# Optimization experiments

Measured on AMD Instinct MI355X. Metric: run time of the kernel, lower is better.

The kernel has to match this reference:

```python
import jax, jax.numpy as jnp
import numpy as np

KSIZE = 3

def setup_inputs() -> dict:
    key = jax.random.key(0)
    k1, k2, k3, k4 = jax.random.split(key, 4)
    B, C, H, W = 4, 64, 256, 512
    x = jax.random.normal(k1, (B, C, H, W), dtype=jnp.float32)
    # precomputed latitude-dependent resampling index into flattened H*W
    idx_flat = jax.random.randint(k2, (KSIZE * H * KSIZE * W,), 0, H * W, dtype=jnp.int64)
    weight = jax.random.normal(k3, (C, C, KSIZE, KSIZE), dtype=jnp.float32) * 0.05
    bias = jax.random.normal(k4, (C,), dtype=jnp.float32) * 0.05
    return {"x": x, "idx_flat": idx_flat, "weight": weight, "bias": bias}

def reference(x, idx_flat, weight, bias):
    B, C, H, W = x.shape
    k = KSIZE
    # latitude-dependent scaled gather: [B, C, H*W] -> [B, C, k*H, k*W]
    x1d = x.reshape(B, C, H * W)
    scaled = jnp.take(x1d, idx_flat, axis=2).reshape(B, C, k * H, k * W)
    # conv with kernel=stride=k, no padding -> [B, C, H, W]
    out = jax.lax.conv_general_dilated(
        scaled, weight,
        window_strides=(k, k), padding='VALID',
        dimension_numbers=('NCHW', 'OIHW', 'NCHW'))
    return out + bias[None, :, None, None]
```

## Files before the change

### kernel.cpp

```cpp
#include <hip/hip_runtime.h>
#include <stdint.h>

#define HW_   131072
#define W_    512
#define C_    64
#define KDIM  576

typedef __bf16 bf16_t;
typedef bf16_t bf16x8 __attribute__((ext_vector_type(8)));
typedef float  f32x4_t __attribute__((ext_vector_type(4)));

__device__ __forceinline__ unsigned short f32_to_bf16(float f) {
    union { float f; unsigned u; } v; v.f = f;
    unsigned r = (v.u + 0x7FFFu + ((v.u >> 16) & 1u)) >> 16;
    return (unsigned short)r;
}

#define XT_BYTES   67108864ull
#define WF_BYTES   73728ull


__global__ __launch_bounds__(256) void k_prep_w(const float* __restrict__ w,
                                                unsigned short* __restrict__ wfrag) {
    int id = blockIdx.x * 256 + threadIdx.x;
    if (id >= 18 * 4 * 64) return;
    int lane = id & 63;
    int nt   = (id >> 6) & 3;
    int kc   = id >> 8;
    int n  = nt * 16 + (lane & 15);
    int k0 = kc * 32 + ((lane >> 4) << 3);
    unsigned short tmp[8];
#pragma unroll
    for (int j = 0; j < 8; ++j) {
        int k = k0 + j;
        int t = k >> 6;
        int c = k & 63;
        tmp[j] = f32_to_bf16(w[(size_t)n * KDIM + c * 9 + t]);
    }
    uint4 v;
    v.x = tmp[0] | ((unsigned)tmp[1] << 16);
    v.y = tmp[2] | ((unsigned)tmp[3] << 16);
    v.z = tmp[4] | ((unsigned)tmp[5] << 16);
    v.w = tmp[6] | ((unsigned)tmp[7] << 16);
    ((uint4*)wfrag)[id] = v;
}

__global__ __launch_bounds__(256) void k_transpose(const float* __restrict__ x,
                                                   unsigned short* __restrict__ xt) {
    int gp = blockIdx.x * 256 + threadIdx.x;
    int b = gp >> 17;
    int p = gp & (HW_ - 1);
    const float* xb = x + ((size_t)b * C_) * HW_ + p;
    uint4* dst = (uint4*)(xt + (size_t)gp * C_);
#pragma unroll
    for (int cc = 0; cc < 8; ++cc) {
        unsigned short tmp[8];
#pragma unroll
        for (int j = 0; j < 8; ++j)
            tmp[j] = f32_to_bf16(xb[(size_t)(cc * 8 + j) * HW_]);
        uint4 v;
        v.x = tmp[0] | ((unsigned)tmp[1] << 16);
        v.y = tmp[2] | ((unsigned)tmp[3] << 16);
        v.z = tmp[4] | ((unsigned)tmp[5] << 16);
        v.w = tmp[6] | ((unsigned)tmp[7] << 16);
        dst[cc] = v;
    }
}

__global__ __launch_bounds__(256) void k_gemm(const unsigned short* __restrict__ xt,
                                              const unsigned short* __restrict__ wfrag,
                                              const int* __restrict__ idx,
                                              const float* __restrict__ bias,
                                              float* __restrict__ out) {
    __shared__ unsigned p_lds[4][64][9];

    int tid  = threadIdx.x;
    int wave = tid >> 6;
    int lane = tid & 63;
    int gbase = blockIdx.x * 256 + wave * 64;
    int b = gbase >> 17;

    {
        int g  = gbase + lane;
        int hw = g & (HW_ - 1);
        int h = hw >> 9, w = hw & (W_ - 1);
        size_t base = (size_t)(3 * h) * (3 * W_) + 3 * w;
#pragma unroll
        for (int th = 0; th < 3; ++th)
#pragma unroll
            for (int tw = 0; tw < 3; ++tw)
                p_lds[wave][lane][th * 3 + tw] = (unsigned)idx[base + (size_t)th * (3 * W_) + tw];
    }
    __syncthreads();

    f32x4_t acc[4][4] = {};
    int quad = lane >> 4;
    int col  = lane & 15;
    const unsigned short* xtb = xt + (((size_t)b) << 17) * C_;

    for (int kc = 0; kc < 18; ++kc) {
        int t = kc >> 1;
        int byteoff = ((kc & 1) << 6) + (quad << 4);

        bf16x8 bfrag[4];
#pragma unroll
        for (int nt = 0; nt < 4; ++nt) {
            const uint4* wp = (const uint4*)(wfrag + ((size_t)((kc * 4 + nt) * 64 + lane) << 3));
            bfrag[nt] = __builtin_bit_cast(bf16x8, *wp);
        }
        bf16x8 afrag[4];
#pragma unroll
        for (int ms = 0; ms < 4; ++ms) {
            unsigned p = p_lds[wave][ms * 16 + col][t];
            const uint4* ap = (const uint4*)((const char*)(xtb + (size_t)p * C_) + byteoff);
            afrag[ms] = __builtin_bit_cast(bf16x8, *ap);
        }
#pragma unroll
        for (int ms = 0; ms < 4; ++ms)
#pragma unroll
            for (int nt = 0; nt < 4; ++nt)
                acc[ms][nt] = __builtin_amdgcn_mfma_f32_16x16x32_bf16(
                    afrag[ms], bfrag[nt], acc[ms][nt], 0, 0, 0);
    }

#pragma unroll
    for (int nt = 0; nt < 4; ++nt) {
        int o = nt * 16 + col;
        float bv = bias[o];
#pragma unroll
        for (int ms = 0; ms < 4; ++ms) {
            int m0 = ms * 16 + quad * 4;
            int hw0 = (gbase + m0) & (HW_ - 1);
            f32x4_t v = acc[ms][nt];
            v.x += bv; v.y += bv; v.z += bv; v.w += bv;
            *(f32x4_t*)(out + (((size_t)(b * 64 + o)) << 17) + hw0) = v;
        }
    }
}

__global__ __launch_bounds__(256) void k_fallback(const float* __restrict__ x,
                                                  const int* __restrict__ idx,
                                                  const float* __restrict__ w,
                                                  const float* __restrict__ bias,
                                                  float* __restrict__ out) {
    size_t g = (size_t)blockIdx.x * 256 + threadIdx.x;
    int hw = (int)(g & (HW_ - 1));
    int o  = (int)((g >> 17) & 63);
    int b  = (int)(g >> 23);
    int h = hw >> 9, ww = hw & (W_ - 1);
    size_t ibase = (size_t)(3 * h) * (3 * W_) + 3 * ww;
    int p[9];
#pragma unroll
    for (int th = 0; th < 3; ++th)
#pragma unroll
        for (int tw = 0; tw < 3; ++tw)
            p[th * 3 + tw] = idx[ibase + (size_t)th * (3 * W_) + tw];
    const float* xb = x + (size_t)b * C_ * HW_;
    const float* wo = w + (size_t)o * KDIM;
    float acc = bias[o];
    for (int c = 0; c < C_; ++c) {
        const float* xc = xb + (size_t)c * HW_;
        const float* wc = wo + c * 9;
#pragma unroll
        for (int t = 0; t < 9; ++t)
            acc += xc[p[t]] * wc[t];
    }
    out[g] = acc;
}

extern "C" void kernel_launch(void* const* d_in, const int* in_sizes, int n_in,
                              void* d_out, int out_size, void* d_ws, size_t ws_size,
                              hipStream_t stream) {
    const float* x    = (const float*)d_in[0];
    const int*   idx  = (const int*)d_in[1];
    const float* w    = (const float*)d_in[2];
    const float* bias = (const float*)d_in[3];
    float* out = (float*)d_out;

    if (ws_size >= XT_BYTES + WF_BYTES) {
        unsigned short* xt    = (unsigned short*)d_ws;
        unsigned short* wfrag = (unsigned short*)((char*)d_ws + XT_BYTES);
        k_prep_w   <<<18,   256, 0, stream>>>(w, wfrag);
        k_transpose<<<2048, 256, 0, stream>>>(x, xt);
        k_gemm     <<<2048, 256, 0, stream>>>(xt, wfrag, idx, bias, out);
    } else {
        k_fallback<<<131072, 256, 0, stream>>>(x, idx, w, bias, out);
    }
}
```

Measured before the change: 375.2 us.

## Stage transpose through LDS and software-pipeline gather loads in GEMM

The transpose kernel now stages a 256-pixel by 64-channel tile in shared memory, so the bf16 channel-last writes become contiguous 16-byte stores rather than strided per-thread stores. The gather-GEMM halves the rows per wave (32 pixels, 128 per block, twice as many blocks) to raise occupancy. It also software-pipelines the gathered A and weight B fragment loads three stages ahead with a fully unrolled K loop, and caches the indices in registers. The cost is more registers for the prefetch buffers, and less weight-fragment reuse per MFMA since each wave now does half as many MFMAs per B load.

```diff
diff --git a/kernel.cpp b/kernel.cpp
--- a/kernel.cpp
+++ b/kernel.cpp
@@ -18,7 +18,6 @@
 
 #define XT_BYTES   67108864ull
 #define WF_BYTES   73728ull
-
 
 __global__ __launch_bounds__(256) void k_prep_w(const float* __restrict__ w,
                                                 unsigned short* __restrict__ wfrag) {
@@ -47,23 +46,31 @@
 
 __global__ __launch_bounds__(256) void k_transpose(const float* __restrict__ x,
                                                    unsigned short* __restrict__ xt) {
-    int gp = blockIdx.x * 256 + threadIdx.x;
-    int b = gp >> 17;
-    int p = gp & (HW_ - 1);
-    const float* xb = x + ((size_t)b * C_) * HW_ + p;
-    uint4* dst = (uint4*)(xt + (size_t)gp * C_);
-#pragma unroll
-    for (int cc = 0; cc < 8; ++cc) {
-        unsigned short tmp[8];
-#pragma unroll
-        for (int j = 0; j < 8; ++j)
-            tmp[j] = f32_to_bf16(xb[(size_t)(cc * 8 + j) * HW_]);
+    __shared__ unsigned short tile[256][68];
+    int t  = threadIdx.x;
+    int gp0 = blockIdx.x * 256;
+    int b  = gp0 >> 17;
+    int p0 = gp0 & (HW_ - 1);
+    const float* xb = x + ((size_t)b * C_) * HW_ + p0 + t;
+#pragma unroll
+    for (int c = 0; c < 64; c += 2) {
+        unsigned a0 = f32_to_bf16(xb[(size_t)c << 17]);
+        unsigned a1 = f32_to_bf16(xb[(size_t)(c + 1) << 17]);
+        *(unsigned*)&tile[t][c] = a0 | (a1 << 16);
+    }
+    __syncthreads();
+    unsigned short* dst = xt + (size_t)gp0 * C_;
+#pragma unroll
+    for (int it = 0; it < 8; ++it) {
+        int cid = it * 256 + t;
+        int px  = cid >> 3;
+        int ch  = cid & 7;
         uint4 v;
-        v.x = tmp[0] | ((unsigned)tmp[1] << 16);
-        v.y = tmp[2] | ((unsigned)tmp[3] << 16);
-        v.z = tmp[4] | ((unsigned)tmp[5] << 16);
-        v.w = tmp[6] | ((unsigned)tmp[7] << 16);
-        dst[cc] = v;
+        v.x = *(unsigned*)&tile[px][ch * 8 + 0];
+        v.y = *(unsigned*)&tile[px][ch * 8 + 2];
+        v.z = *(unsigned*)&tile[px][ch * 8 + 4];
+        v.w = *(unsigned*)&tile[px][ch * 8 + 6];
+        ((uint4*)(dst + (size_t)px * C_))[ch] = v;
     }
 }
 
@@ -72,65 +79,89 @@
                                               const int* __restrict__ idx,
                                               const float* __restrict__ bias,
                                               float* __restrict__ out) {
-    __shared__ unsigned p_lds[4][64][9];
+    __shared__ unsigned p_lds[128][9];
 
     int tid  = threadIdx.x;
     int wave = tid >> 6;
     int lane = tid & 63;
-    int gbase = blockIdx.x * 256 + wave * 64;
+    int gbase = blockIdx.x * 128;
     int b = gbase >> 17;
 
     {
-        int g  = gbase + lane;
+        int px   = tid >> 1;
+        int half = tid & 1;
+        int g  = gbase + px;
         int hw = g & (HW_ - 1);
         int h = hw >> 9, w = hw & (W_ - 1);
         size_t base = (size_t)(3 * h) * (3 * W_) + 3 * w;
-#pragma unroll
-        for (int th = 0; th < 3; ++th)
-#pragma unroll
-            for (int tw = 0; tw < 3; ++tw)
-                p_lds[wave][lane][th * 3 + tw] = (unsigned)idx[base + (size_t)th * (3 * W_) + tw];
+        if (half == 0) {
+#pragma unroll
+            for (int t = 0; t < 5; ++t)
+                p_lds[px][t] = (unsigned)idx[base + (size_t)(t / 3) * (3 * W_) + (t % 3)];
+        } else {
+#pragma unroll
+            for (int t = 5; t < 9; ++t)
+                p_lds[px][t] = (unsigned)idx[base + (size_t)(t / 3) * (3 * W_) + (t % 3)];
+        }
     }
     __syncthreads();
 
-    f32x4_t acc[4][4] = {};
     int quad = lane >> 4;
     int col  = lane & 15;
+    int pxw  = wave * 32;
+
+    unsigned p_reg[9][2];
+#pragma unroll
+    for (int t = 0; t < 9; ++t) {
+        p_reg[t][0] = p_lds[pxw + col][t];
+        p_reg[t][1] = p_lds[pxw + 16 + col][t];
+    }
+
     const unsigned short* xtb = xt + (((size_t)b) << 17) * C_;
-
-    for (int kc = 0; kc < 18; ++kc) {
-        int t = kc >> 1;
-        int byteoff = ((kc & 1) << 6) + (quad << 4);
-
-        bf16x8 bfrag[4];
-#pragma unroll
-        for (int nt = 0; nt < 4; ++nt) {
-            const uint4* wp = (const uint4*)(wfrag + ((size_t)((kc * 4 + nt) * 64 + lane) << 3));
-            bfrag[nt] = __builtin_bit_cast(bf16x8, *wp);
-        }
-        bf16x8 afrag[4];
-#pragma unroll
-        for (int ms = 0; ms < 4; ++ms) {
-            unsigned p = p_lds[wave][ms * 16 + col][t];
-            const uint4* ap = (const uint4*)((const char*)(xtb + (size_t)p * C_) + byteoff);
-            afrag[ms] = __builtin_bit_cast(bf16x8, *ap);
-        }
-#pragma unroll
-        for (int ms = 0; ms < 4; ++ms)
+    const uint4* wf = (const uint4*)wfrag;
+
+    f32x4_t acc[2][4] = {};
+    bf16x8 Abuf[3][2];
+    bf16x8 Bbuf[3][4];
+
+#define ISSUE(s, slot)                                                              \
+    {                                                                               \
+        const int t_ = (s) >> 1, h_ = (s) & 1;                                      \
+        _Pragma("unroll")                                                           \
+        for (int ms = 0; ms < 2; ++ms) {                                            \
+            const uint4* ap = (const uint4*)((const char*)xtb +                     \
+                ((size_t)p_reg[t_][ms] << 7) + (h_ << 6) + (quad << 4));            \
+            Abuf[slot][ms] = __builtin_bit_cast(bf16x8, *ap);                       \
+        }                                                                           \
+        _Pragma("unroll")                                                           \
+        for (int nt = 0; nt < 4; ++nt)                                              \
+            Bbuf[slot][nt] = __builtin_bit_cast(bf16x8, wf[((s) * 4 + nt) * 64 + lane]); \
+    }
+
+    ISSUE(0, 0)
+    ISSUE(1, 1)
+    ISSUE(2, 2)
+#pragma unroll
+    for (int s = 0; s < 18; ++s) {
+        const int slot = s % 3;
+#pragma unroll
+        for (int ms = 0; ms < 2; ++ms)
 #pragma unroll
             for (int nt = 0; nt < 4; ++nt)
                 acc[ms][nt] = __builtin_amdgcn_mfma_f32_16x16x32_bf16(
-                    afrag[ms], bfrag[nt], acc[ms][nt], 0, 0, 0);
-    }
+                    Abuf[slot][ms], Bbuf[slot][nt], acc[ms][nt], 0, 0, 0);
+        if (s + 3 < 18) ISSUE(s + 3, slot)
+    }
+#undef ISSUE
 
 #pragma unroll
     for (int nt = 0; nt < 4; ++nt) {
         int o = nt * 16 + col;
         float bv = bias[o];
 #pragma unroll
-        for (int ms = 0; ms < 4; ++ms) {
+        for (int ms = 0; ms < 2; ++ms) {
             int m0 = ms * 16 + quad * 4;
-            int hw0 = (gbase + m0) & (HW_ - 1);
+            int hw0 = (gbase + pxw + m0) & (HW_ - 1);
             f32x4_t v = acc[ms][nt];
             v.x += bv; v.y += bv; v.z += bv; v.w += bv;
             *(f32x4_t*)(out + (((size_t)(b * 64 + o)) << 17) + hw0) = v;
@@ -182,7 +213,7 @@
         unsigned short* wfrag = (unsigned short*)((char*)d_ws + XT_BYTES);
         k_prep_w   <<<18,   256, 0, stream>>>(w, wfrag);
         k_transpose<<<2048, 256, 0, stream>>>(x, xt);
-        k_gemm     <<<2048, 256, 0, stream>>>(xt, wfrag, idx, bias, out);
+        k_gemm     <<<4096, 256, 0, stream>>>(xt, wfrag, idx, bias, out);
     } else {
         k_fallback<<<131072, 256, 0, stream>>>(x, idx, w, bias, out);
     }
```

Result: faster. 354.8 us (-5.4%).
